# Performance work log

Hardware: AMD Instinct MI355X
Metric: run time of the kernel (lower is better)

## Reference

```python
import jax, jax.numpy as jnp
import numpy as np

B, T, D_MODEL, D_HIDDEN, MAX_SEQLEN = 4, 2048, 1024, 256, 2048


def setup_inputs() -> dict:
    key = jax.random.key(0)
    ks = jax.random.split(key, 8)
    s_in = 1.0 / np.sqrt(D_MODEL)
    s_out = 1.0 / np.sqrt(D_HIDDEN)
    # xavier_uniform bound for W_bias (fan_in = fan_out = MAX_SEQLEN)
    xb = np.sqrt(6.0 / (MAX_SEQLEN + MAX_SEQLEN))
    return {
        "q": jax.random.normal(ks[0], (B, T, D_MODEL), jnp.float32),
        "k": jax.random.normal(ks[1], (B, T, D_MODEL), jnp.float32),
        "v": jax.random.normal(ks[2], (B, T, D_MODEL), jnp.float32),
        "Wq": jax.random.normal(ks[3], (D_MODEL, D_HIDDEN), jnp.float32) * s_in,
        "Wk": jax.random.normal(ks[4], (D_MODEL, D_HIDDEN), jnp.float32) * s_in,
        "Wv": jax.random.normal(ks[5], (D_MODEL, D_HIDDEN), jnp.float32) * s_in,
        "Wo": jax.random.normal(ks[6], (D_HIDDEN, D_MODEL), jnp.float32) * s_out,
        "W_bias": jax.random.uniform(ks[7], (MAX_SEQLEN, MAX_SEQLEN), jnp.float32, -xb, xb),
    }


def reference(q, k, v, Wq, Wk, Wv, Wo, W_bias):
    Ti, Tj = q.shape[1], k.shape[1]
    Q = q @ Wq                      # [B,Ti,dh]
    K = k @ Wk                      # [B,Tj,dh]
    V = v @ Wv                      # [B,Tj,dh]
    pos_bias = W_bias[:Ti, :Tj][None]               # [1,Ti,Tj]
    # NOTE: source subtracts max over dim 0 (batch). For pos_bias that dim is 1,
    # so exp_pos_bias == exp(0) == ones -- reproduced faithfully here.
    max_key = jnp.max(K, axis=0, keepdims=True)      # [1,Tj,dh]
    max_pos_bias = jnp.max(pos_bias, axis=0, keepdims=True)
    exp_key = jnp.exp(K - max_key)                   # [B,Tj,dh]
    exp_pos_bias = jnp.exp(pos_bias - max_pos_bias)  # [1,Ti,Tj]
    num = jnp.einsum('ij,bjd->bid', exp_pos_bias[0], exp_key * V)  # [B,Ti,dh]
    den = jnp.einsum('ij,bjd->bid', exp_pos_bias[0], exp_key)      # [B,Ti,dh]
    Yt = jax.nn.sigmoid(Q) * num / den
    return Yt @ Wo                  # [B,Ti,d_model]
```

## Files before the change

### kernel.cpp

```cpp
#include <hip/hip_runtime.h>
#include <hip/hip_bf16.h>
#include <math.h>

#define B_   4
#define T_   2048
#define DM   1024
#define DH   256
#define M_   (B_*T_)

typedef __bf16 bf16;
typedef __attribute__((ext_vector_type(8))) __bf16 bf16x8;
typedef __attribute__((ext_vector_type(4))) float  f32x4;

#define LDT 72

__device__ inline float sigmoidf_(float x) { return 1.0f / (1.0f + __expf(-x)); }

__global__ void transpose_cvt(const float* __restrict__ in, bf16* __restrict__ out,
                              int R, int C) {
    __shared__ float tile[32][33];
    int c0 = blockIdx.x * 32, r0 = blockIdx.y * 32;
    int tx = threadIdx.x & 31, ty = threadIdx.x >> 5;
    #pragma unroll
    for (int i = ty; i < 32; i += 8)
        tile[i][tx] = in[(long)(r0 + i) * C + c0 + tx];
    __syncthreads();
    #pragma unroll
    for (int i = ty; i < 32; i += 8)
        out[(long)(c0 + i) * R + r0 + tx] = (bf16)tile[tx][i];
}

__global__ __launch_bounds__(256)
void gemm_proj(const float* __restrict__ qin, const float* __restrict__ kin,
               const float* __restrict__ vin,
               const bf16* __restrict__ Wq_t, const bf16* __restrict__ Wk_t,
               const bf16* __restrict__ Wv_t,
               bf16* __restrict__ Qb, bf16* __restrict__ Kb, bf16* __restrict__ Vb)
{
    __shared__ __align__(16) bf16 As[64][LDT];
    __shared__ __align__(16) bf16 Bs[64][LDT];

    const int z = blockIdx.z;
    const float* A  = (z == 0) ? qin  : (z == 1) ? kin  : vin;
    const bf16*  Wt = (z == 0) ? Wq_t : (z == 1) ? Wk_t : Wv_t;
    bf16*        C  = (z == 0) ? Qb   : (z == 1) ? Kb   : Vb;

    const int m0 = blockIdx.x * 64;
    const int n0 = blockIdx.y * 64;
    const int tid = threadIdx.x, lane = tid & 63, wave = tid >> 6;
    const int wr = wave >> 1, wc = wave & 1;
    const int q4 = lane >> 4, l16 = lane & 15;

    f32x4 acc[2][2] = {};
    const int srow = tid >> 3, scol = (tid & 7) * 8;

    for (int k0 = 0; k0 < DM; k0 += 64) {
        #pragma unroll
        for (int h = 0; h < 2; ++h) {
            int row = srow + 32 * h;
            const float* src = &A[(long)(m0 + row) * DM + k0 + scol];
            f32x4 x0 = *(const f32x4*)src;
            f32x4 x1 = *(const f32x4*)(src + 4);
            bf16x8 o;
            #pragma unroll
            for (int e = 0; e < 4; ++e) { o[e] = (bf16)x0[e]; o[4 + e] = (bf16)x1[e]; }
            *(bf16x8*)&As[row][scol] = o;
            *(bf16x8*)&Bs[row][scol] = *(const bf16x8*)&Wt[(long)(n0 + row) * DM + k0 + scol];
        }
        __syncthreads();
        #pragma unroll
        for (int kk = 0; kk < 64; kk += 32) {
            bf16x8 a0 = *(const bf16x8*)&As[wr * 32      + l16][kk + q4 * 8];
            bf16x8 a1 = *(const bf16x8*)&As[wr * 32 + 16 + l16][kk + q4 * 8];
            bf16x8 b0 = *(const bf16x8*)&Bs[wc * 32      + l16][kk + q4 * 8];
            bf16x8 b1 = *(const bf16x8*)&Bs[wc * 32 + 16 + l16][kk + q4 * 8];
            acc[0][0] = __builtin_amdgcn_mfma_f32_16x16x32_bf16(a0, b0, acc[0][0], 0, 0, 0);
            acc[0][1] = __builtin_amdgcn_mfma_f32_16x16x32_bf16(a0, b1, acc[0][1], 0, 0, 0);
            acc[1][0] = __builtin_amdgcn_mfma_f32_16x16x32_bf16(a1, b0, acc[1][0], 0, 0, 0);
            acc[1][1] = __builtin_amdgcn_mfma_f32_16x16x32_bf16(a1, b1, acc[1][1], 0, 0, 0);
        }
        __syncthreads();
    }
    #pragma unroll
    for (int i = 0; i < 2; ++i)
        #pragma unroll
        for (int j = 0; j < 2; ++j)
            #pragma unroll
            for (int r = 0; r < 4; ++r) {
                int gm = m0 + wr * 32 + i * 16 + q4 * 4 + r;
                int gn = n0 + wc * 32 + j * 16 + l16;
                C[(long)gm * DH + gn] = (bf16)acc[i][j][r];
            }
}

__global__ void reduce_kv(const bf16* __restrict__ Kb, const bf16* __restrict__ Vb,
                          float* __restrict__ numb, float* __restrict__ denb)
{
    const int d  = threadIdx.x;
    const int j0 = blockIdx.x * 8;
    float sn[B_] = {0.f, 0.f, 0.f, 0.f};
    float sd[B_] = {0.f, 0.f, 0.f, 0.f};
    for (int jj = 0; jj < 8; ++jj) {
        int j = j0 + jj;
        float kv[B_], vv[B_], mx = -INFINITY;
        #pragma unroll
        for (int b = 0; b < B_; ++b) {
            kv[b] = (float)Kb[((long)b * T_ + j) * DH + d];
            vv[b] = (float)Vb[((long)b * T_ + j) * DH + d];
            mx = fmaxf(mx, kv[b]);
        }
        #pragma unroll
        for (int b = 0; b < B_; ++b) {
            float e = __expf(kv[b] - mx);
            sn[b] += e * vv[b];
            sd[b] += e;
        }
    }
    #pragma unroll
    for (int b = 0; b < B_; ++b) {
        atomicAdd(&numb[b * DH + d], sn[b]);
        atomicAdd(&denb[b * DH + d], sd[b]);
    }
}

__global__ __launch_bounds__(256)
void gemm_out(const bf16* __restrict__ Qb, const bf16* __restrict__ Wo_t,
              const float* __restrict__ numb, const float* __restrict__ denb,
              float* __restrict__ out)
{
    __shared__ __align__(16) bf16 As[64][LDT];
    __shared__ __align__(16) bf16 Bs[64][LDT];

    const int m0 = blockIdx.x * 64;
    const int n0 = blockIdx.y * 64;
    const int b  = blockIdx.x >> 5;
    const int tid = threadIdx.x, lane = tid & 63, wave = tid >> 6;
    const int wr = wave >> 1, wc = wave & 1;
    const int q4 = lane >> 4, l16 = lane & 15;

    f32x4 acc[2][2] = {};
    const int srow = tid >> 3, scol = (tid & 7) * 8;

    for (int k0 = 0; k0 < DH; k0 += 64) {
        f32x4 rn0 = *(const f32x4*)&numb[b * DH + k0 + scol];
        f32x4 rn1 = *(const f32x4*)&numb[b * DH + k0 + scol + 4];
        f32x4 rd0 = *(const f32x4*)&denb[b * DH + k0 + scol];
        f32x4 rd1 = *(const f32x4*)&denb[b * DH + k0 + scol + 4];
        float rv[8];
        #pragma unroll
        for (int e = 0; e < 4; ++e) { rv[e] = rn0[e] / rd0[e]; rv[4 + e] = rn1[e] / rd1[e]; }

        #pragma unroll
        for (int h = 0; h < 2; ++h) {
            int row = srow + 32 * h;
            bf16x8 xq = *(const bf16x8*)&Qb[(long)(m0 + row) * DH + k0 + scol];
            bf16x8 o;
            #pragma unroll
            for (int e = 0; e < 8; ++e)
                o[e] = (bf16)(sigmoidf_((float)xq[e]) * rv[e]);
            *(bf16x8*)&As[row][scol] = o;
            *(bf16x8*)&Bs[row][scol] = *(const bf16x8*)&Wo_t[(long)(n0 + row) * DH + k0 + scol];
        }
        __syncthreads();
        #pragma unroll
        for (int kk = 0; kk < 64; kk += 32) {
            bf16x8 a0 = *(const bf16x8*)&As[wr * 32      + l16][kk + q4 * 8];
            bf16x8 a1 = *(const bf16x8*)&As[wr * 32 + 16 + l16][kk + q4 * 8];
            bf16x8 b0 = *(const bf16x8*)&Bs[wc * 32      + l16][kk + q4 * 8];
            bf16x8 b1 = *(const bf16x8*)&Bs[wc * 32 + 16 + l16][kk + q4 * 8];
            acc[0][0] = __builtin_amdgcn_mfma_f32_16x16x32_bf16(a0, b0, acc[0][0], 0, 0, 0);
            acc[0][1] = __builtin_amdgcn_mfma_f32_16x16x32_bf16(a0, b1, acc[0][1], 0, 0, 0);
            acc[1][0] = __builtin_amdgcn_mfma_f32_16x16x32_bf16(a1, b0, acc[1][0], 0, 0, 0);
            acc[1][1] = __builtin_amdgcn_mfma_f32_16x16x32_bf16(a1, b1, acc[1][1], 0, 0, 0);
        }
        __syncthreads();
    }
    #pragma unroll
    for (int i = 0; i < 2; ++i)
        #pragma unroll
        for (int j = 0; j < 2; ++j)
            #pragma unroll
            for (int r = 0; r < 4; ++r) {
                int gm = m0 + wr * 32 + i * 16 + q4 * 4 + r;
                int gn = n0 + wc * 32 + j * 16 + l16;
                out[(long)gm * DM + gn] = acc[i][j][r];
            }
}

extern "C" void kernel_launch(void* const* d_in, const int* in_sizes, int n_in,
                              void* d_out, int out_size, void* d_ws, size_t ws_size,
                              hipStream_t stream)
{
    const float* q  = (const float*)d_in[0];
    const float* k  = (const float*)d_in[1];
    const float* v  = (const float*)d_in[2];
    const float* Wq = (const float*)d_in[3];
    const float* Wk = (const float*)d_in[4];
    const float* Wv = (const float*)d_in[5];
    const float* Wo = (const float*)d_in[6];
    float* out = (float*)d_out;

    char* ws = (char*)d_ws;
    bf16* Qb    = (bf16*)ws;  ws += (size_t)M_ * DH * sizeof(bf16);
    bf16* Kb    = (bf16*)ws;  ws += (size_t)M_ * DH * sizeof(bf16);
    bf16* Vb    = (bf16*)ws;  ws += (size_t)M_ * DH * sizeof(bf16);
    bf16* Wq_t  = (bf16*)ws;  ws += (size_t)DM * DH * sizeof(bf16);
    bf16* Wk_t  = (bf16*)ws;  ws += (size_t)DM * DH * sizeof(bf16);
    bf16* Wv_t  = (bf16*)ws;  ws += (size_t)DM * DH * sizeof(bf16);
    bf16* Wo_t  = (bf16*)ws;  ws += (size_t)DM * DH * sizeof(bf16);
    float* numb = (float*)ws; ws += (size_t)B_ * DH * sizeof(float);
    float* denb = (float*)ws; ws += (size_t)B_ * DH * sizeof(float);

    transpose_cvt<<<dim3(DH / 32, DM / 32), 256, 0, stream>>>(Wq, Wq_t, DM, DH);
    transpose_cvt<<<dim3(DH / 32, DM / 32), 256, 0, stream>>>(Wk, Wk_t, DM, DH);
    transpose_cvt<<<dim3(DH / 32, DM / 32), 256, 0, stream>>>(Wv, Wv_t, DM, DH);
    transpose_cvt<<<dim3(DM / 32, DH / 32), 256, 0, stream>>>(Wo, Wo_t, DH, DM);

    hipMemsetAsync(numb, 0, 2 * (size_t)B_ * DH * sizeof(float), stream);

    gemm_proj<<<dim3(M_ / 64, DH / 64, 3), 256, 0, stream>>>(q, k, v, Wq_t, Wk_t, Wv_t,
                                                             Qb, Kb, Vb);
    reduce_kv<<<256, 256, 0, stream>>>(Kb, Vb, numb, denb);
    gemm_out<<<dim3(M_ / 64, DM / 64), 256, 0, stream>>>(Qb, Wo_t, numb, denb, out);
}
```

Baseline: 226.3 us.

## Widen GEMM N-tiles to 128, merge weight transposes, precompute num/den ratio in LDS

Both GEMMs now use 64x128 output tiles, so each wave computes 2x4 MFMA tiles. This halves how often the fp32 activation A-tile is re-read and converted per output column, and raises MFMA work per LDS load. The four weight-transpose launches are merged into a single launch. gemm_out computes num/den once per block into shared memory instead of redoing the divisions in every k-step. The cost is more registers and LDS per block, plus half as many blocks in the grid, which may reduce occupancy and load balance.

Result: faster. 208.7 us (-7.8%).

```diff
diff --git a/kernel.cpp b/kernel.cpp
--- a/kernel.cpp
+++ b/kernel.cpp
@@ -9,6 +9,7 @@
 #define M_   (B_*T_)
 
 typedef __bf16 bf16;
+typedef __attribute__((ext_vector_type(4))) __bf16 bf16x4;
 typedef __attribute__((ext_vector_type(8))) __bf16 bf16x8;
 typedef __attribute__((ext_vector_type(4))) float  f32x4;
 
@@ -16,11 +17,21 @@
 
 __device__ inline float sigmoidf_(float x) { return 1.0f / (1.0f + __expf(-x)); }
 
-__global__ void transpose_cvt(const float* __restrict__ in, bf16* __restrict__ out,
-                              int R, int C) {
+__global__ void transpose_cvt_all(const float* __restrict__ Wq, const float* __restrict__ Wk,
+                                  const float* __restrict__ Wv, const float* __restrict__ Wo,
+                                  bf16* __restrict__ Wq_t, bf16* __restrict__ Wk_t,
+                                  bf16* __restrict__ Wv_t, bf16* __restrict__ Wo_t)
+{
     __shared__ float tile[32][33];
-    int c0 = blockIdx.x * 32, r0 = blockIdx.y * 32;
-    int tx = threadIdx.x & 31, ty = threadIdx.x >> 5;
+    const int bid = blockIdx.x;
+    const int w = bid >> 8, t = bid & 255;
+    const float* in; bf16* out; int R, C, sh;
+    if      (w == 0) { in = Wq; out = Wq_t; R = DM; C = DH; sh = 3; }
+    else if (w == 1) { in = Wk; out = Wk_t; R = DM; C = DH; sh = 3; }
+    else if (w == 2) { in = Wv; out = Wv_t; R = DM; C = DH; sh = 3; }
+    else             { in = Wo; out = Wo_t; R = DH; C = DM; sh = 5; }
+    const int r0 = (t >> sh) * 32, c0 = (t & ((1 << sh) - 1)) * 32;
+    const int tx = threadIdx.x & 31, ty = threadIdx.x >> 5;
     #pragma unroll
     for (int i = ty; i < 32; i += 8)
         tile[i][tx] = in[(long)(r0 + i) * C + c0 + tx];
@@ -30,7 +41,7 @@
         out[(long)(c0 + i) * R + r0 + tx] = (bf16)tile[tx][i];
 }
 
-__global__ __launch_bounds__(256)
+__global__ __launch_bounds__(256, 4)
 void gemm_proj(const float* __restrict__ qin, const float* __restrict__ kin,
                const float* __restrict__ vin,
                const bf16* __restrict__ Wq_t, const bf16* __restrict__ Wk_t,
@@ -38,7 +49,7 @@
                bf16* __restrict__ Qb, bf16* __restrict__ Kb, bf16* __restrict__ Vb)
 {
     __shared__ __align__(16) bf16 As[64][LDT];
-    __shared__ __align__(16) bf16 Bs[64][LDT];
+    __shared__ __align__(16) bf16 Bs[128][LDT];
 
     const int z = blockIdx.z;
     const float* A  = (z == 0) ? qin  : (z == 1) ? kin  : vin;
@@ -46,49 +57,54 @@
     bf16*        C  = (z == 0) ? Qb   : (z == 1) ? Kb   : Vb;
 
     const int m0 = blockIdx.x * 64;
-    const int n0 = blockIdx.y * 64;
+    const int n0 = blockIdx.y * 128;
     const int tid = threadIdx.x, lane = tid & 63, wave = tid >> 6;
     const int wr = wave >> 1, wc = wave & 1;
     const int q4 = lane >> 4, l16 = lane & 15;
 
-    f32x4 acc[2][2] = {};
-    const int srow = tid >> 3, scol = (tid & 7) * 8;
+    f32x4 acc[2][4] = {};
+    const int ar = tid >> 2, ac4 = (tid & 3) * 4;
+    const int br = tid >> 1, bc8 = (tid & 1) * 8;
 
     for (int k0 = 0; k0 < DM; k0 += 64) {
-        #pragma unroll
-        for (int h = 0; h < 2; ++h) {
-            int row = srow + 32 * h;
-            const float* src = &A[(long)(m0 + row) * DM + k0 + scol];
-            f32x4 x0 = *(const f32x4*)src;
-            f32x4 x1 = *(const f32x4*)(src + 4);
-            bf16x8 o;
-            #pragma unroll
-            for (int e = 0; e < 4; ++e) { o[e] = (bf16)x0[e]; o[4 + e] = (bf16)x1[e]; }
-            *(bf16x8*)&As[row][scol] = o;
-            *(bf16x8*)&Bs[row][scol] = *(const bf16x8*)&Wt[(long)(n0 + row) * DM + k0 + scol];
-        }
+        const float* ap = &A[(long)(m0 + ar) * DM + k0];
+        #pragma unroll
+        for (int i = 0; i < 4; ++i) {
+            f32x4 x = *(const f32x4*)(ap + ac4 + 16 * i);
+            bf16x4 o;
+            #pragma unroll
+            for (int e = 0; e < 4; ++e) o[e] = (bf16)x[e];
+            *(bf16x4*)&As[ar][ac4 + 16 * i] = o;
+        }
+        const bf16* bp = &Wt[(long)(n0 + br) * DM + k0];
+        #pragma unroll
+        for (int i = 0; i < 4; ++i)
+            *(bf16x8*)&Bs[br][bc8 + 16 * i] = *(const bf16x8*)(bp + bc8 + 16 * i);
         __syncthreads();
         #pragma unroll
         for (int kk = 0; kk < 64; kk += 32) {
             bf16x8 a0 = *(const bf16x8*)&As[wr * 32      + l16][kk + q4 * 8];
             bf16x8 a1 = *(const bf16x8*)&As[wr * 32 + 16 + l16][kk + q4 * 8];
-            bf16x8 b0 = *(const bf16x8*)&Bs[wc * 32      + l16][kk + q4 * 8];
-            bf16x8 b1 = *(const bf16x8*)&Bs[wc * 32 + 16 + l16][kk + q4 * 8];
-            acc[0][0] = __builtin_amdgcn_mfma_f32_16x16x32_bf16(a0, b0, acc[0][0], 0, 0, 0);
-            acc[0][1] = __builtin_amdgcn_mfma_f32_16x16x32_bf16(a0, b1, acc[0][1], 0, 0, 0);
-            acc[1][0] = __builtin_amdgcn_mfma_f32_16x16x32_bf16(a1, b0, acc[1][0], 0, 0, 0);
-            acc[1][1] = __builtin_amdgcn_mfma_f32_16x16x32_bf16(a1, b1, acc[1][1], 0, 0, 0);
+            bf16x8 bf[4];
+            #pragma unroll
+            for (int j = 0; j < 4; ++j)
+                bf[j] = *(const bf16x8*)&Bs[wc * 64 + j * 16 + l16][kk + q4 * 8];
+            #pragma unroll
+            for (int j = 0; j < 4; ++j) {
+                acc[0][j] = __builtin_amdgcn_mfma_f32_16x16x32_bf16(a0, bf[j], acc[0][j], 0, 0, 0);
+                acc[1][j] = __builtin_amdgcn_mfma_f32_16x16x32_bf16(a1, bf[j], acc[1][j], 0, 0, 0);
+            }
         }
         __syncthreads();
     }
     #pragma unroll
     for (int i = 0; i < 2; ++i)
         #pragma unroll
-        for (int j = 0; j < 2; ++j)
+        for (int j = 0; j < 4; ++j)
             #pragma unroll
             for (int r = 0; r < 4; ++r) {
                 int gm = m0 + wr * 32 + i * 16 + q4 * 4 + r;
-                int gn = n0 + wc * 32 + j * 16 + l16;
+                int gn = n0 + wc * 64 + j * 16 + l16;
                 C[(long)gm * DH + gn] = (bf16)acc[i][j][r];
             }
 }
@@ -123,66 +139,70 @@
     }
 }
 
-__global__ __launch_bounds__(256)
+__global__ __launch_bounds__(256, 4)
 void gemm_out(const bf16* __restrict__ Qb, const bf16* __restrict__ Wo_t,
               const float* __restrict__ numb, const float* __restrict__ denb,
               float* __restrict__ out)
 {
     __shared__ __align__(16) bf16 As[64][LDT];
-    __shared__ __align__(16) bf16 Bs[64][LDT];
+    __shared__ __align__(16) bf16 Bs[128][LDT];
+    __shared__ float rv_s[DH];
 
     const int m0 = blockIdx.x * 64;
-    const int n0 = blockIdx.y * 64;
+    const int n0 = blockIdx.y * 128;
     const int b  = blockIdx.x >> 5;
     const int tid = threadIdx.x, lane = tid & 63, wave = tid >> 6;
     const int wr = wave >> 1, wc = wave & 1;
     const int q4 = lane >> 4, l16 = lane & 15;
 
-    f32x4 acc[2][2] = {};
-    const int srow = tid >> 3, scol = (tid & 7) * 8;
+    rv_s[tid] = numb[b * DH + tid] / denb[b * DH + tid];
+    __syncthreads();
+
+    f32x4 acc[2][4] = {};
+    const int ar = tid >> 2, ac8 = (tid & 3) * 8;
+    const int br = tid >> 1, bc8 = (tid & 1) * 8;
 
     for (int k0 = 0; k0 < DH; k0 += 64) {
-        f32x4 rn0 = *(const f32x4*)&numb[b * DH + k0 + scol];
-        f32x4 rn1 = *(const f32x4*)&numb[b * DH + k0 + scol + 4];
-        f32x4 rd0 = *(const f32x4*)&denb[b * DH + k0 + scol];
-        f32x4 rd1 = *(const f32x4*)&denb[b * DH + k0 + scol + 4];
-        float rv[8];
-        #pragma unroll
-        for (int e = 0; e < 4; ++e) { rv[e] = rn0[e] / rd0[e]; rv[4 + e] = rn1[e] / rd1[e]; }
-
-        #pragma unroll
-        for (int h = 0; h < 2; ++h) {
-            int row = srow + 32 * h;
-            bf16x8 xq = *(const bf16x8*)&Qb[(long)(m0 + row) * DH + k0 + scol];
+        const bf16* qp = &Qb[(long)(m0 + ar) * DH + k0];
+        #pragma unroll
+        for (int i = 0; i < 2; ++i) {
+            int c = ac8 + 32 * i;
+            bf16x8 xq = *(const bf16x8*)(qp + c);
             bf16x8 o;
             #pragma unroll
             for (int e = 0; e < 8; ++e)
-                o[e] = (bf16)(sigmoidf_((float)xq[e]) * rv[e]);
-            *(bf16x8*)&As[row][scol] = o;
-            *(bf16x8*)&Bs[row][scol] = *(const bf16x8*)&Wo_t[(long)(n0 + row) * DH + k0 + scol];
-        }
+                o[e] = (bf16)(sigmoidf_((float)xq[e]) * rv_s[k0 + c + e]);
+            *(bf16x8*)&As[ar][c] = o;
+        }
+        const bf16* wp = &Wo_t[(long)(n0 + br) * DH + k0];
+        #pragma unroll
+        for (int i = 0; i < 4; ++i)
+            *(bf16x8*)&Bs[br][bc8 + 16 * i] = *(const bf16x8*)(wp + bc8 + 16 * i);
         __syncthreads();
         #pragma unroll
         for (int kk = 0; kk < 64; kk += 32) {
             bf16x8 a0 = *(const bf16x8*)&As[wr * 32      + l16][kk + q4 * 8];
             bf16x8 a1 = *(const bf16x8*)&As[wr * 32 + 16 + l16][kk + q4 * 8];
-            bf16x8 b0 = *(const bf16x8*)&Bs[wc * 32      + l16][kk + q4 * 8];
-            bf16x8 b1 = *(const bf16x8*)&Bs[wc * 32 + 16 + l16][kk + q4 * 8];
-            acc[0][0] = __builtin_amdgcn_mfma_f32_16x16x32_bf16(a0, b0, acc[0][0], 0, 0, 0);
-            acc[0][1] = __builtin_amdgcn_mfma_f32_16x16x32_bf16(a0, b1, acc[0][1], 0, 0, 0);
-            acc[1][0] = __builtin_amdgcn_mfma_f32_16x16x32_bf16(a1, b0, acc[1][0], 0, 0, 0);
-            acc[1][1] = __builtin_amdgcn_mfma_f32_16x16x32_bf16(a1, b1, acc[1][1], 0, 0, 0);
+            bf16x8 bf[4];
+            #pragma unroll
+            for (int j = 0; j < 4; ++j)
+                bf[j] = *(const bf16x8*)&Bs[wc * 64 + j * 16 + l16][kk + q4 * 8];
+            #pragma unroll
+            for (int j = 0; j < 4; ++j) {
+                acc[0][j] = __builtin_amdgcn_mfma_f32_16x16x32_bf16(a0, bf[j], acc[0][j], 0, 0, 0);
+                acc[1][j] = __builtin_amdgcn_mfma_f32_16x16x32_bf16(a1, bf[j], acc[1][j], 0, 0, 0);
+            }
         }
         __syncthreads();
     }
     #pragma unroll
     for (int i = 0; i < 2; ++i)
         #pragma unroll
-        for (int j = 0; j < 2; ++j)
+        for (int j = 0; j < 4; ++j)
             #pragma unroll
             for (int r = 0; r < 4; ++r) {
                 int gm = m0 + wr * 32 + i * 16 + q4 * 4 + r;
-                int gn = n0 + wc * 32 + j * 16 + l16;
+                int gn = n0 + wc * 64 + j * 16 + l16;
                 out[(long)gm * DM + gn] = acc[i][j][r];
             }
 }
@@ -211,15 +231,11 @@
     float* numb = (float*)ws; ws += (size_t)B_ * DH * sizeof(float);
     float* denb = (float*)ws; ws += (size_t)B_ * DH * sizeof(float);
 
-    transpose_cvt<<<dim3(DH / 32, DM / 32), 256, 0, stream>>>(Wq, Wq_t, DM, DH);
-    transpose_cvt<<<dim3(DH / 32, DM / 32), 256, 0, stream>>>(Wk, Wk_t, DM, DH);
-    transpose_cvt<<<dim3(DH / 32, DM / 32), 256, 0, stream>>>(Wv, Wv_t, DM, DH);
-    transpose_cvt<<<dim3(DM / 32, DH / 32), 256, 0, stream>>>(Wo, Wo_t, DH, DM);
-
+    transpose_cvt_all<<<1024, 256, 0, stream>>>(Wq, Wk, Wv, Wo, Wq_t, Wk_t, Wv_t, Wo_t);
     hipMemsetAsync(numb, 0, 2 * (size_t)B_ * DH * sizeof(float), stream);
 
-    gemm_proj<<<dim3(M_ / 64, DH / 64, 3), 256, 0, stream>>>(q, k, v, Wq_t, Wk_t, Wv_t,
-                                                             Qb, Kb, Vb);
+    gemm_proj<<<dim3(M_ / 64, DH / 128, 3), 256, 0, stream>>>(q, k, v, Wq_t, Wk_t, Wv_t,
+                                                              Qb, Kb, Vb);
     reduce_kv<<<256, 256, 0, stream>>>(Kb, Vb, numb, denb);
-    gemm_out<<<dim3(M_ / 64, DM / 64), 256, 0, stream>>>(Qb, Wo_t, numb, denb, out);
-}
+    gemm_out<<<dim3(M_ / 64, DM / 128), 256, 0, stream>>>(Qb, Wo_t, numb, denb, out);
+}
```
